# Optimization experiments

Measured on AMD Instinct MI355X. Metric: run time of the kernel, lower is better.

## Reference

```python
import jax, jax.numpy as jnp
import numpy as np

B, S, D, H = 2, 2048, 1024, 16
DK = D // H  # 64


def setup_inputs() -> dict:
    key = jax.random.key(0)
    ks = jax.random.split(key, 11)
    scale = 1.0 / np.sqrt(D)
    inp = {
        "x": jax.random.normal(ks[0], (B, S, D), dtype=jnp.float32),
        "z": jax.random.normal(ks[1], (B, S, D), dtype=jnp.float32),
        # causal mask, broadcast over batch and heads; masked_fill where mask==0
        "mask": jnp.tril(jnp.ones((1, 1, S, S), dtype=jnp.int32)),
        "wq_w": jax.random.normal(ks[2], (D, D), dtype=jnp.float32) * scale,
        "wq_b": jax.random.normal(ks[3], (D,), dtype=jnp.float32) * 0.01,
        "wk_w": jax.random.normal(ks[4], (D, D), dtype=jnp.float32) * scale,
        "wk_b": jax.random.normal(ks[5], (D,), dtype=jnp.float32) * 0.01,
        "wv_w": jax.random.normal(ks[6], (D, D), dtype=jnp.float32) * scale,
        "wv_b": jax.random.normal(ks[7], (D,), dtype=jnp.float32) * 0.01,
        "wo_w": jax.random.normal(ks[8], (D, D), dtype=jnp.float32) * scale,
        "wo_b": jax.random.normal(ks[9], (D,), dtype=jnp.float32) * 0.01,
    }
    return inp


def reference(x, z, mask, wq_w, wq_b, wk_w, wk_b, wv_w, wv_b, wo_w, wo_b):
    # torch Linear: y = x @ W.T + b
    q = x @ wq_w.T + wq_b
    k = z @ wk_w.T + wk_b
    # NOTE: faithful to source bug: value uses wk, not wv (wv is a dead param)
    v = z @ wk_w.T + wk_b

    def split_heads(t):  # [B,S,D] -> [B,H,S,DK]
        return t.reshape(B, S, H, DK).transpose(0, 2, 1, 3)

    q, k, v = split_heads(q), split_heads(k), split_heads(v)

    scores = jnp.einsum("bhqd,bhkd->bhqk", q, k) * (DK ** -0.5)
    scores = jnp.where(mask == 0, -jnp.inf, scores)
    attn_weights = jax.nn.softmax(scores, axis=-1)  # [B,H,S,S]
    atn = jnp.einsum("bhqk,bhkd->bhqd", attn_weights, v)

    concat = atn.transpose(0, 2, 1, 3).reshape(B, S, D)
    output = concat @ wo_w.T + wo_b  # dropout rate 0.0 -> identity
    concat_attn_weight = attn_weights.sum(axis=1)  # [B,S,S]
    return output, concat_attn_weight
```

## Files before the change

### kernel.cpp

```cpp
#include <hip/hip_runtime.h>

typedef __bf16 bf16_t;
typedef __bf16 bf16x4 __attribute__((ext_vector_type(4)));
typedef __bf16 bf16x8 __attribute__((ext_vector_type(8)));
typedef float  f32x4  __attribute__((ext_vector_type(4)));

#define MFMA(a, b, c) __builtin_amdgcn_mfma_f32_16x16x32_bf16((a), (b), (c), 0, 0, 0)

static constexpr int Bsz = 2, S = 2048, D = 1024, H = 16, DK = 64;
#define QSCALE 0.18033688011112042f

__global__ __launch_bounds__(256) void cvt5(
    const float* __restrict__ x, const float* __restrict__ z,
    const float* __restrict__ wq, const float* __restrict__ wk,
    const float* __restrict__ wo,
    bf16_t* __restrict__ xb, bf16_t* __restrict__ zb,
    bf16_t* __restrict__ wqb, bf16_t* __restrict__ wkb, bf16_t* __restrict__ wob)
{
    constexpr int NXZ = Bsz * S * D / 4;
    constexpr int NW  = D * D / 4;
    int i = blockIdx.x * 256 + threadIdx.x;
    const float* s; bf16_t* d; int off;
    if (i < NXZ)                 { s = x;  d = xb;  off = i; }
    else if (i < 2 * NXZ)        { s = z;  d = zb;  off = i - NXZ; }
    else if (i < 2 * NXZ + NW)   { s = wq; d = wqb; off = i - 2 * NXZ; }
    else if (i < 2 * NXZ + 2*NW) { s = wk; d = wkb; off = i - 2 * NXZ - NW; }
    else                         { s = wo; d = wob; off = i - 2 * NXZ - 2 * NW; }
    float4 v = *(const float4*)&s[(size_t)off * 4];
    bf16x4 o;
    o[0] = (bf16_t)v.x; o[1] = (bf16_t)v.y; o[2] = (bf16_t)v.z; o[3] = (bf16_t)v.w;
    *(bf16x4*)&d[(size_t)off * 4] = o;
}

__global__ __launch_bounds__(512) void gemm_qk(
    const bf16_t* __restrict__ xA, const bf16_t* __restrict__ wqB,
    const float* __restrict__ wqb, bf16_t* __restrict__ Qc,
    const bf16_t* __restrict__ zA, const bf16_t* __restrict__ wkB,
    const float* __restrict__ wkb, bf16_t* __restrict__ Kc,
    bf16_t* __restrict__ KTout)
{
    constexpr int N = D, K = D;
    const int zi = blockIdx.z;
    const bf16_t* A    = zi ? zA  : xA;
    const bf16_t* B    = zi ? wkB : wqB;
    const float*  bias = zi ? wkb : wqb;
    bf16_t*       C    = zi ? Kc  : Qc;
    const float   sc   = zi ? 1.f : QSCALE;

    __shared__ bf16_t As[2][128][40];
    __shared__ bf16_t Bs[2][128][40];

    const int t    = threadIdx.x;
    const int wave = t >> 6, lane = t & 63;
    const int quad = lane >> 4, l15 = lane & 15;
    const int wm = (wave >> 1) * 32, wn = (wave & 1) * 64;
    const int rowbase = blockIdx.y * 128, colbase = blockIdx.x * 128;
    const int r  = t >> 2;
    const int cc = (t & 3) << 3;

    f32x4 acc[2][4];
#pragma unroll
    for (int i = 0; i < 2; ++i)
#pragma unroll
        for (int j = 0; j < 4; ++j) acc[i][j] = {0.f, 0.f, 0.f, 0.f};

    bf16x8 areg = *(const bf16x8*)&A[(size_t)(rowbase + r) * K + cc];
    bf16x8 breg = *(const bf16x8*)&B[(size_t)(colbase + r) * K + cc];
    *(bf16x8*)&As[0][r][cc] = areg;
    *(bf16x8*)&Bs[0][r][cc] = breg;
    __syncthreads();

    for (int kt = 0; kt < K; kt += 32) {
        const int cur = (kt >> 5) & 1, nxt = cur ^ 1;
        const bool more = (kt + 32) < K;
        if (more) {
            areg = *(const bf16x8*)&A[(size_t)(rowbase + r) * K + kt + 32 + cc];
            breg = *(const bf16x8*)&B[(size_t)(colbase + r) * K + kt + 32 + cc];
        }

        bf16x8 af[2], bfr[4];
#pragma unroll
        for (int mt = 0; mt < 2; ++mt)
            af[mt] = *(const bf16x8*)&As[cur][wm + mt * 16 + l15][quad * 8];
#pragma unroll
        for (int nt = 0; nt < 4; ++nt)
            bfr[nt] = *(const bf16x8*)&Bs[cur][wn + nt * 16 + l15][quad * 8];
#pragma unroll
        for (int mt = 0; mt < 2; ++mt)
#pragma unroll
            for (int nt = 0; nt < 4; ++nt)
                acc[mt][nt] = MFMA(af[mt], bfr[nt], acc[mt][nt]);

        if (more) {
            *(bf16x8*)&As[nxt][r][cc] = areg;
            *(bf16x8*)&Bs[nxt][r][cc] = breg;
        }
        __syncthreads();
    }

#pragma unroll
    for (int nt = 0; nt < 4; ++nt) {
        int col  = colbase + wn + nt * 16 + l15;
        float bv = bias[col];
#pragma unroll
        for (int mt = 0; mt < 2; ++mt) {
            int row0 = rowbase + wm + mt * 16 + quad * 4;
#pragma unroll
            for (int rr = 0; rr < 4; ++rr) {
                float v = (acc[mt][nt][rr] + bv) * sc;
                C[(size_t)(row0 + rr) * N + col] = (bf16_t)v;
                if (zi) {
                    int row = row0 + rr;
                    int bb = row >> 11, srow = row & (S - 1);
                    int hh = col >> 6,  dd   = col & 63;
                    KTout[(((size_t)bb * H + hh) * DK + dd) * S + srow] = (bf16_t)v;
                }
            }
        }
    }
}

__global__ __launch_bounds__(256) void gemm_obt(
    const bf16_t* __restrict__ A, const bf16_t* __restrict__ B,
    const float* __restrict__ bias, float* __restrict__ C)
{
    constexpr int N = D, K = D;
    __shared__ bf16_t As[2][64][40];
    __shared__ bf16_t Bs[2][128][40];

    const int t    = threadIdx.x;
    const int wave = t >> 6, lane = t & 63;
    const int quad = lane >> 4, l15 = lane & 15;
    const int wm = (wave >> 1) * 32, wn = (wave & 1) * 64;
    const int rowbase = blockIdx.y * 64, colbase = blockIdx.x * 128;
    const int r  = t >> 2;
    const int cc = (t & 3) << 3;

    f32x4 acc[2][4];
#pragma unroll
    for (int i = 0; i < 2; ++i)
#pragma unroll
        for (int j = 0; j < 4; ++j) acc[i][j] = {0.f, 0.f, 0.f, 0.f};

    bf16x8 areg = *(const bf16x8*)&A[(size_t)(rowbase + r) * K + cc];
    bf16x8 breg0 = *(const bf16x8*)&B[(size_t)(colbase + r) * K + cc];
    bf16x8 breg1 = *(const bf16x8*)&B[(size_t)(colbase + 64 + r) * K + cc];
    *(bf16x8*)&As[0][r][cc]      = areg;
    *(bf16x8*)&Bs[0][r][cc]      = breg0;
    *(bf16x8*)&Bs[0][64 + r][cc] = breg1;
    __syncthreads();

    for (int kt = 0; kt < K; kt += 32) {
        const int cur = (kt >> 5) & 1, nxt = cur ^ 1;
        const bool more = (kt + 32) < K;
        if (more) {
            areg  = *(const bf16x8*)&A[(size_t)(rowbase + r) * K + kt + 32 + cc];
            breg0 = *(const bf16x8*)&B[(size_t)(colbase + r) * K + kt + 32 + cc];
            breg1 = *(const bf16x8*)&B[(size_t)(colbase + 64 + r) * K + kt + 32 + cc];
        }

        bf16x8 af[2], bfr[4];
#pragma unroll
        for (int mt = 0; mt < 2; ++mt)
            af[mt] = *(const bf16x8*)&As[cur][wm + mt * 16 + l15][quad * 8];
#pragma unroll
        for (int nt = 0; nt < 4; ++nt)
            bfr[nt] = *(const bf16x8*)&Bs[cur][wn + nt * 16 + l15][quad * 8];
#pragma unroll
        for (int mt = 0; mt < 2; ++mt)
#pragma unroll
            for (int nt = 0; nt < 4; ++nt)
                acc[mt][nt] = MFMA(af[mt], bfr[nt], acc[mt][nt]);

        if (more) {
            *(bf16x8*)&As[nxt][r][cc]      = areg;
            *(bf16x8*)&Bs[nxt][r][cc]      = breg0;
            *(bf16x8*)&Bs[nxt][64 + r][cc] = breg1;
        }
        __syncthreads();
    }

#pragma unroll
    for (int nt = 0; nt < 4; ++nt) {
        int col  = colbase + wn + nt * 16 + l15;
        float bv = bias[col];
#pragma unroll
        for (int mt = 0; mt < 2; ++mt) {
            int row0 = rowbase + wm + mt * 16 + quad * 4;
#pragma unroll
            for (int rr = 0; rr < 4; ++rr)
                C[(size_t)(row0 + rr) * N + col] = acc[mt][nt][rr] + bv;
        }
    }
}

__global__ __launch_bounds__(256) void attn_flash(
    const bf16_t* __restrict__ Q, const bf16_t* __restrict__ Km,
    const bf16_t* __restrict__ KT,
    bf16_t* __restrict__ Oc, float* __restrict__ m_ws, float* __restrict__ il_ws)
{
    const int h = blockIdx.y, b = blockIdx.z;
    const int t = threadIdx.x;
    const int wave = t >> 6, lane = t & 63;
    const int quad = lane >> 4, l15 = lane & 15;

    __shared__ bf16_t Ks[2][64][72];
    __shared__ bf16_t KTs[2][64][72];
    __shared__ bf16_t PQ[64][72];

    const int hcol = h * DK;
    const bf16_t* KTh = KT + ((size_t)(b * H + h)) * DK * S;
    const size_t bS = (size_t)b * S;

    const int jr = (t >> 3);
    const int ce = (t & 7) * 8;
    const int iloc = wave * 16 + l15;

    for (int half = 0; half < 2; ++half) {
        const int qt = half == 0 ? (int)blockIdx.x : 31 - (int)blockIdx.x;
        const size_t qrow0 = bS + (size_t)qt * 64;

        __syncthreads();
        bf16x8 qld[2], kreg[2], ktreg[2];
#pragma unroll
        for (int p = 0; p < 2; ++p) {
            qld[p]   = *(const bf16x8*)&Q[(qrow0 + p * 32 + jr) * D + hcol + ce];
            kreg[p]  = *(const bf16x8*)&Km[(bS + p * 32 + jr) * D + hcol + ce];
            ktreg[p] = *(const bf16x8*)&KTh[(size_t)(p * 32 + jr) * S + ce];
        }
#pragma unroll
        for (int p = 0; p < 2; ++p) {
            *(bf16x8*)&PQ[p * 32 + jr][ce]     = qld[p];
            *(bf16x8*)&Ks[0][p * 32 + jr][ce]  = kreg[p];
            *(bf16x8*)&KTs[0][p * 32 + jr][ce] = ktreg[p];
        }
        __syncthreads();
        const bf16x8 qf0 = *(const bf16x8*)&PQ[wave * 16 + l15][quad * 8];
        const bf16x8 qf1 = *(const bf16x8*)&PQ[wave * 16 + l15][32 + quad * 8];

        f32x4 accO[4];
#pragma unroll
        for (int u = 0; u < 4; ++u) accO[u] = {0.f, 0.f, 0.f, 0.f};
        float m_cur = -1e30f, l_cur = 0.f;

        auto softmax_pv = [&](f32x4 sv[4], int cur) {
            float tm = sv[0][0];
#pragma unroll
            for (int nt = 0; nt < 4; ++nt)
#pragma unroll
                for (int r = 0; r < 4; ++r) tm = fmaxf(tm, sv[nt][r]);
            tm = fmaxf(tm, __shfl_xor(tm, 16));
            tm = fmaxf(tm, __shfl_xor(tm, 32));
            if (__any(tm > m_cur + 8.f)) {
                float m_new = fmaxf(m_cur, tm);
                float alpha = exp2f(m_cur - m_new);
                m_cur = m_new;
                l_cur *= alpha;
                float alpha4[4];
#pragma unroll
                for (int r = 0; r < 4; ++r)
                    alpha4[r] = __shfl(alpha, (quad << 4) + quad * 4 + r, 64);
#pragma unroll
                for (int u = 0; u < 4; ++u)
#pragma unroll
                    for (int r = 0; r < 4; ++r) accO[u][r] *= alpha4[r];
            }
            float rs = 0.f;
#pragma unroll
            for (int nt = 0; nt < 4; ++nt)
#pragma unroll
                for (int r = 0; r < 4; ++r) {
                    float p = exp2f(sv[nt][r] - m_cur);
                    sv[nt][r] = p;
                    rs += p;
                }
            rs += __shfl_xor(rs, 16);
            rs += __shfl_xor(rs, 32);
            l_cur += rs;

#pragma unroll
            for (int nt = 0; nt < 4; ++nt) {
                bf16x4 pk;
                pk[0] = (bf16_t)sv[nt][0]; pk[1] = (bf16_t)sv[nt][1];
                pk[2] = (bf16_t)sv[nt][2]; pk[3] = (bf16_t)sv[nt][3];
                *(bf16x4*)&PQ[wave * 16 + l15][nt * 16 + quad * 4] = pk;
            }
            asm volatile("s_waitcnt lgkmcnt(0)" ::: "memory");

            bf16x8 pa0 = *(const bf16x8*)&PQ[wave * 16 + l15][quad * 8];
            bf16x8 pa1 = *(const bf16x8*)&PQ[wave * 16 + l15][32 + quad * 8];
            __builtin_amdgcn_s_setprio(1);
#pragma unroll
            for (int u = 0; u < 4; ++u) {
                bf16x8 v0 = *(const bf16x8*)&KTs[cur][u * 16 + l15][quad * 8];
                bf16x8 v1 = *(const bf16x8*)&KTs[cur][u * 16 + l15][32 + quad * 8];
                accO[u] = MFMA(pa0, v0, accO[u]);
                accO[u] = MFMA(pa1, v1, accO[u]);
            }
            __builtin_amdgcn_s_setprio(0);
        };

        for (int jt = 0; jt < qt; ++jt) {
            const int cur = jt & 1, nxt = cur ^ 1;
#pragma unroll
            for (int p = 0; p < 2; ++p) {
                kreg[p]  = *(const bf16x8*)&Km[(bS + (size_t)(jt + 1) * 64 + p * 32 + jr) * D + hcol + ce];
                ktreg[p] = *(const bf16x8*)&KTh[(size_t)(p * 32 + jr) * S + (size_t)(jt + 1) * 64 + ce];
            }

            f32x4 sv[4];
            __builtin_amdgcn_s_setprio(1);
#pragma unroll
            for (int nt = 0; nt < 4; ++nt) {
                bf16x8 a0 = *(const bf16x8*)&Ks[cur][nt * 16 + l15][quad * 8];
                bf16x8 a1 = *(const bf16x8*)&Ks[cur][nt * 16 + l15][32 + quad * 8];
                f32x4 a = {0.f, 0.f, 0.f, 0.f};
                a = MFMA(a0, qf0, a);
                a = MFMA(a1, qf1, a);
                sv[nt] = a;
            }
            __builtin_amdgcn_s_setprio(0);
            softmax_pv(sv, cur);

#pragma unroll
            for (int p = 0; p < 2; ++p) {
                *(bf16x8*)&Ks[nxt][p * 32 + jr][ce]  = kreg[p];
                *(bf16x8*)&KTs[nxt][p * 32 + jr][ce] = ktreg[p];
            }
            __syncthreads();
        }

        {
            const int cur = qt & 1;
            f32x4 sv[4];
            __builtin_amdgcn_s_setprio(1);
#pragma unroll
            for (int nt = 0; nt < 4; ++nt) {
                bf16x8 a0 = *(const bf16x8*)&Ks[cur][nt * 16 + l15][quad * 8];
                bf16x8 a1 = *(const bf16x8*)&Ks[cur][nt * 16 + l15][32 + quad * 8];
                f32x4 a = {0.f, 0.f, 0.f, 0.f};
                a = MFMA(a0, qf0, a);
                a = MFMA(a1, qf1, a);
#pragma unroll
                for (int r = 0; r < 4; ++r)
                    if ((nt * 16 + quad * 4 + r) > iloc) a[r] = -1e30f;
                sv[nt] = a;
            }
            __builtin_amdgcn_s_setprio(0);
            softmax_pv(sv, cur);
        }

        float invl = 1.f / l_cur;
        float invl4[4];
#pragma unroll
        for (int r = 0; r < 4; ++r)
            invl4[r] = __shfl(invl, (quad << 4) + quad * 4 + r, 64);
#pragma unroll
        for (int u = 0; u < 4; ++u)
#pragma unroll
            for (int r = 0; r < 4; ++r)
                Oc[(qrow0 + wave * 16 + quad * 4 + r) * D + hcol + u * 16 + l15] =
                    (bf16_t)(accO[u][r] * invl4[r]);

        if (quad == 0) {
            size_t sb = ((size_t)(b * H + h)) * S + (size_t)qt * 64 + wave * 16 + l15;
            m_ws[sb]  = m_cur;
            il_ws[sb] = invl;
        }
    }
}

__global__ __launch_bounds__(256) void attn_wsum(
    const bf16_t* __restrict__ Q, const bf16_t* __restrict__ Km,
    const float* __restrict__ m_ws, const float* __restrict__ il_ws,
    float* __restrict__ out2)
{
    const int jt = blockIdx.x, qt = blockIdx.y, b = blockIdx.z;
    const int t  = threadIdx.x;
    float* tile = out2 + (size_t)b * S * S + (size_t)qt * 64 * S + (size_t)jt * 64;

    if (jt > qt) {
        int r0 = t >> 2, c0 = (t & 3) * 16;
#pragma unroll
        for (int e = 0; e < 16; ++e) tile[(size_t)r0 * S + c0 + e] = 0.f;
        return;
    }

    const int wave = t >> 6, lane = t & 63;
    const int quad = lane >> 4, l15 = lane & 15;
    __shared__ bf16_t Ks[2][64][72];
    __shared__ bf16_t Qs[2][64][72];

    const int jr = (t >> 3), ce = (t & 7) * 8;
    const size_t krow = (size_t)b * S + (size_t)jt * 64;
    const size_t qrow = (size_t)b * S + (size_t)qt * 64;

    f32x4 accs[4];
#pragma unroll
    for (int nt = 0; nt < 4; ++nt) accs[nt] = {0.f, 0.f, 0.f, 0.f};

    bf16x8 kreg[2], qreg[2];
#pragma unroll
    for (int p = 0; p < 2; ++p) {
        kreg[p] = *(const bf16x8*)&Km[(krow + p * 32 + jr) * D + ce];
        qreg[p] = *(const bf16x8*)&Q[(qrow + p * 32 + jr) * D + ce];
    }
#pragma unroll
    for (int p = 0; p < 2; ++p) {
        *(bf16x8*)&Ks[0][p * 32 + jr][ce] = kreg[p];
        *(bf16x8*)&Qs[0][p * 32 + jr][ce] = qreg[p];
    }
    __syncthreads();

    const size_t mlb0 = (size_t)(b * H) * S + (size_t)qt * 64 + wave * 16 + quad * 4;

    if (jt < qt) {
        for (int h = 0; h < H; ++h) {
            const int cur = h & 1, nxt = cur ^ 1;
            if (h < H - 1) {
                const int hc = (h + 1) * DK;
#pragma unroll
                for (int p = 0; p < 2; ++p) {
                    kreg[p] = *(const bf16x8*)&Km[(krow + p * 32 + jr) * D + hc + ce];
                    qreg[p] = *(const bf16x8*)&Q[(qrow + p * 32 + jr) * D + hc + ce];
                }
            }

            bf16x8 qf0 = *(const bf16x8*)&Qs[cur][wave * 16 + l15][quad * 8];
            bf16x8 qf1 = *(const bf16x8*)&Qs[cur][wave * 16 + l15][32 + quad * 8];
            f32x4 mr = *(const f32x4*)&m_ws[mlb0 + (size_t)h * S];
            f32x4 il = *(const f32x4*)&il_ws[mlb0 + (size_t)h * S];

#pragma unroll
            for (int nt = 0; nt < 4; ++nt) {
                bf16x8 k0 = *(const bf16x8*)&Ks[cur][nt * 16 + l15][quad * 8];
                bf16x8 k1 = *(const bf16x8*)&Ks[cur][nt * 16 + l15][32 + quad * 8];
                f32x4 a = {0.f, 0.f, 0.f, 0.f};
                a = MFMA(qf0, k0, a);
                a = MFMA(qf1, k1, a);
#pragma unroll
                for (int r = 0; r < 4; ++r)
                    accs[nt][r] = fmaf(exp2f(a[r] - mr[r]), il[r], accs[nt][r]);
            }

            if (h < H - 1) {
#pragma unroll
                for (int p = 0; p < 2; ++p) {
                    *(bf16x8*)&Ks[nxt][p * 32 + jr][ce] = kreg[p];
                    *(bf16x8*)&Qs[nxt][p * 32 + jr][ce] = qreg[p];
                }
            }
            __syncthreads();
        }
    } else {
        for (int h = 0; h < H; ++h) {
            const int cur = h & 1, nxt = cur ^ 1;
            if (h < H - 1) {
                const int hc = (h + 1) * DK;
#pragma unroll
                for (int p = 0; p < 2; ++p) {
                    kreg[p] = *(const bf16x8*)&Km[(krow + p * 32 + jr) * D + hc + ce];
                    qreg[p] = *(const bf16x8*)&Q[(qrow + p * 32 + jr) * D + hc + ce];
                }
            }

            bf16x8 qf0 = *(const bf16x8*)&Qs[cur][wave * 16 + l15][quad * 8];
            bf16x8 qf1 = *(const bf16x8*)&Qs[cur][wave * 16 + l15][32 + quad * 8];
            f32x4 mr = *(const f32x4*)&m_ws[mlb0 + (size_t)h * S];
            f32x4 il = *(const f32x4*)&il_ws[mlb0 + (size_t)h * S];

#pragma unroll
            for (int nt = 0; nt < 4; ++nt) {
                bf16x8 k0 = *(const bf16x8*)&Ks[cur][nt * 16 + l15][quad * 8];
                bf16x8 k1 = *(const bf16x8*)&Ks[cur][nt * 16 + l15][32 + quad * 8];
                f32x4 a = {0.f, 0.f, 0.f, 0.f};
                a = MFMA(qf0, k0, a);
                a = MFMA(qf1, k1, a);
#pragma unroll
                for (int r = 0; r < 4; ++r) {
                    int i = wave * 16 + quad * 4 + r;
                    int j = nt * 16 + l15;
                    float p = (j <= i) ? exp2f(a[r] - mr[r]) * il[r] : 0.f;
                    accs[nt][r] += p;
                }
            }

            if (h < H - 1) {
#pragma unroll
                for (int p = 0; p < 2; ++p) {
                    *(bf16x8*)&Ks[nxt][p * 32 + jr][ce] = kreg[p];
                    *(bf16x8*)&Qs[nxt][p * 32 + jr][ce] = qreg[p];
                }
            }
            __syncthreads();
        }
    }

#pragma unroll
    for (int nt = 0; nt < 4; ++nt)
#pragma unroll
        for (int r = 0; r < 4; ++r)
            tile[(size_t)(wave * 16 + quad * 4 + r) * S + nt * 16 + l15] = accs[nt][r];
}

extern "C" void kernel_launch(void* const* d_in, const int* in_sizes, int n_in,
                              void* d_out, int out_size, void* d_ws, size_t ws_size,
                              hipStream_t stream)
{
    const float* x    = (const float*)d_in[0];
    const float* z    = (const float*)d_in[1];
    const float* wq_w = (const float*)d_in[3];
    const float* wq_b = (const float*)d_in[4];
    const float* wk_w = (const float*)d_in[5];
    const float* wk_b = (const float*)d_in[6];
    const float* wo_w = (const float*)d_in[9];
    const float* wo_b = (const float*)d_in[10];

    float* out  = (float*)d_out;
    float* out2 = out + (size_t)Bsz * S * D;

    float*  m_ws  = (float*)d_ws;
    float*  il_ws = m_ws + (size_t)Bsz * H * S;
    bf16_t* Qws   = (bf16_t*)(il_ws + (size_t)Bsz * H * S);
    bf16_t* Kws   = Qws + (size_t)Bsz * S * D;
    bf16_t* wq_bf = Kws + (size_t)Bsz * S * D;
    bf16_t* wk_bf = wq_bf + (size_t)D * D;
    bf16_t* wo_bf = wk_bf + (size_t)D * D;
    bf16_t* xb    = (bf16_t*)out;
    bf16_t* zb    = xb + (size_t)Bsz * S * D;
    bf16_t* Cc    = (bf16_t*)out2;
    bf16_t* KTws  = Cc + (size_t)Bsz * S * D;

    constexpr int CVT_BLOCKS = (2 * (Bsz * S * D / 4) + 3 * (D * D / 4)) / 256;
    cvt5<<<dim3(CVT_BLOCKS), dim3(256), 0, stream>>>(
        x, z, wq_w, wk_w, wo_w, xb, zb, wq_bf, wk_bf, wo_bf);
    gemm_qk<<<dim3(D / 128, (Bsz * S) / 128, 2), dim3(512), 0, stream>>>(
        xb, wq_bf, wq_b, Qws, zb, wk_bf, wk_b, Kws, KTws);
    attn_flash<<<dim3(S / 128, H, Bsz), dim3(256), 0, stream>>>(
        Qws, Kws, KTws, Cc, m_ws, il_ws);
    gemm_obt<<<dim3(D / 128, (Bsz * S) / 64, 1), dim3(256), 0, stream>>>(
        Cc, wo_bf, wo_b, out);
    attn_wsum<<<dim3(S / 64, S / 64, Bsz), dim3(256), 0, stream>>>(
        Qws, Kws, m_ws, il_ws, out2);
}
```

Measured before the change: 271.1 us.

## Process both paired query tiles in one KV sweep sharing loaded K tiles

The flash attention kernel previously handled its two causal-balanced query tiles (qt and 31-qt) one after the other, streaming K/V tiles from global memory twice. It now keeps two sets of accumulators and softmax state and walks the K/V sequence once, computing both tiles' scores from the same shared-memory K tile and running tile A only while it is causally active. This cuts global K/V loads and barriers, at the cost of more registers per thread and a second shared P buffer, which may reduce occupancy.

After: 275.8 us. About the same (+1.7%).

```diff
diff --git a/kernel.cpp b/kernel.cpp
--- a/kernel.cpp
+++ b/kernel.cpp
@@ -206,7 +206,8 @@
 
     __shared__ bf16_t Ks[2][64][72];
     __shared__ bf16_t KTs[2][64][72];
-    __shared__ bf16_t PQ[64][72];
+    __shared__ bf16_t PA[64][72];
+    __shared__ bf16_t PB[64][72];
 
     const int hcol = h * DK;
     const bf16_t* KTh = KT + ((size_t)(b * H + h)) * DK * S;
@@ -216,141 +217,156 @@
     const int ce = (t & 7) * 8;
     const int iloc = wave * 16 + l15;
 
-    for (int half = 0; half < 2; ++half) {
-        const int qt = half == 0 ? (int)blockIdx.x : 31 - (int)blockIdx.x;
-        const size_t qrow0 = bS + (size_t)qt * 64;
-
-        __syncthreads();
-        bf16x8 qld[2], kreg[2], ktreg[2];
-#pragma unroll
-        for (int p = 0; p < 2; ++p) {
-            qld[p]   = *(const bf16x8*)&Q[(qrow0 + p * 32 + jr) * D + hcol + ce];
-            kreg[p]  = *(const bf16x8*)&Km[(bS + p * 32 + jr) * D + hcol + ce];
-            ktreg[p] = *(const bf16x8*)&KTh[(size_t)(p * 32 + jr) * S + ce];
-        }
-#pragma unroll
-        for (int p = 0; p < 2; ++p) {
-            *(bf16x8*)&PQ[p * 32 + jr][ce]     = qld[p];
-            *(bf16x8*)&Ks[0][p * 32 + jr][ce]  = kreg[p];
-            *(bf16x8*)&KTs[0][p * 32 + jr][ce] = ktreg[p];
-        }
-        __syncthreads();
-        const bf16x8 qf0 = *(const bf16x8*)&PQ[wave * 16 + l15][quad * 8];
-        const bf16x8 qf1 = *(const bf16x8*)&PQ[wave * 16 + l15][32 + quad * 8];
-
-        f32x4 accO[4];
-#pragma unroll
-        for (int u = 0; u < 4; ++u) accO[u] = {0.f, 0.f, 0.f, 0.f};
-        float m_cur = -1e30f, l_cur = 0.f;
-
-        auto softmax_pv = [&](f32x4 sv[4], int cur) {
-            float tm = sv[0][0];
-#pragma unroll
-            for (int nt = 0; nt < 4; ++nt)
-#pragma unroll
-                for (int r = 0; r < 4; ++r) tm = fmaxf(tm, sv[nt][r]);
-            tm = fmaxf(tm, __shfl_xor(tm, 16));
-            tm = fmaxf(tm, __shfl_xor(tm, 32));
-            if (__any(tm > m_cur + 8.f)) {
-                float m_new = fmaxf(m_cur, tm);
-                float alpha = exp2f(m_cur - m_new);
-                m_cur = m_new;
-                l_cur *= alpha;
-                float alpha4[4];
-#pragma unroll
-                for (int r = 0; r < 4; ++r)
-                    alpha4[r] = __shfl(alpha, (quad << 4) + quad * 4 + r, 64);
-#pragma unroll
-                for (int u = 0; u < 4; ++u)
-#pragma unroll
-                    for (int r = 0; r < 4; ++r) accO[u][r] *= alpha4[r];
-            }
-            float rs = 0.f;
-#pragma unroll
-            for (int nt = 0; nt < 4; ++nt)
-#pragma unroll
-                for (int r = 0; r < 4; ++r) {
-                    float p = exp2f(sv[nt][r] - m_cur);
-                    sv[nt][r] = p;
-                    rs += p;
-                }
-            rs += __shfl_xor(rs, 16);
-            rs += __shfl_xor(rs, 32);
-            l_cur += rs;
-
-#pragma unroll
-            for (int nt = 0; nt < 4; ++nt) {
-                bf16x4 pk;
-                pk[0] = (bf16_t)sv[nt][0]; pk[1] = (bf16_t)sv[nt][1];
-                pk[2] = (bf16_t)sv[nt][2]; pk[3] = (bf16_t)sv[nt][3];
-                *(bf16x4*)&PQ[wave * 16 + l15][nt * 16 + quad * 4] = pk;
-            }
-            asm volatile("s_waitcnt lgkmcnt(0)" ::: "memory");
-
-            bf16x8 pa0 = *(const bf16x8*)&PQ[wave * 16 + l15][quad * 8];
-            bf16x8 pa1 = *(const bf16x8*)&PQ[wave * 16 + l15][32 + quad * 8];
-            __builtin_amdgcn_s_setprio(1);
-#pragma unroll
-            for (int u = 0; u < 4; ++u) {
-                bf16x8 v0 = *(const bf16x8*)&KTs[cur][u * 16 + l15][quad * 8];
-                bf16x8 v1 = *(const bf16x8*)&KTs[cur][u * 16 + l15][32 + quad * 8];
-                accO[u] = MFMA(pa0, v0, accO[u]);
-                accO[u] = MFMA(pa1, v1, accO[u]);
-            }
-            __builtin_amdgcn_s_setprio(0);
-        };
-
-        for (int jt = 0; jt < qt; ++jt) {
-            const int cur = jt & 1, nxt = cur ^ 1;
+    const int qtA = (int)blockIdx.x;
+    const int qtB = 31 - qtA;
+    const size_t qrowA = bS + (size_t)qtA * 64;
+    const size_t qrowB = bS + (size_t)qtB * 64;
+
+    bf16x8 qldA[2], qldB[2], kreg[2], ktreg[2];
+#pragma unroll
+    for (int p = 0; p < 2; ++p) {
+        qldA[p]  = *(const bf16x8*)&Q[(qrowA + p * 32 + jr) * D + hcol + ce];
+        qldB[p]  = *(const bf16x8*)&Q[(qrowB + p * 32 + jr) * D + hcol + ce];
+        kreg[p]  = *(const bf16x8*)&Km[(bS + p * 32 + jr) * D + hcol + ce];
+        ktreg[p] = *(const bf16x8*)&KTh[(size_t)(p * 32 + jr) * S + ce];
+    }
+#pragma unroll
+    for (int p = 0; p < 2; ++p) {
+        *(bf16x8*)&PA[p * 32 + jr][ce]     = qldA[p];
+        *(bf16x8*)&PB[p * 32 + jr][ce]     = qldB[p];
+        *(bf16x8*)&Ks[0][p * 32 + jr][ce]  = kreg[p];
+        *(bf16x8*)&KTs[0][p * 32 + jr][ce] = ktreg[p];
+    }
+    __syncthreads();
+    const bf16x8 qfA0 = *(const bf16x8*)&PA[wave * 16 + l15][quad * 8];
+    const bf16x8 qfA1 = *(const bf16x8*)&PA[wave * 16 + l15][32 + quad * 8];
+    const bf16x8 qfB0 = *(const bf16x8*)&PB[wave * 16 + l15][quad * 8];
+    const bf16x8 qfB1 = *(const bf16x8*)&PB[wave * 16 + l15][32 + quad * 8];
+
+    f32x4 accA[4], accB[4];
+#pragma unroll
+    for (int u = 0; u < 4; ++u) { accA[u] = {0.f, 0.f, 0.f, 0.f}; accB[u] = {0.f, 0.f, 0.f, 0.f}; }
+    float mA = -1e30f, lA = 0.f, mB = -1e30f, lB = 0.f;
+
+    auto softmax_pv = [&](f32x4 (&sv)[4], int cur, float& m_cur, float& l_cur,
+                          f32x4 (&accO)[4], bf16_t (&P)[64][72]) {
+        float tm = sv[0][0];
+#pragma unroll
+        for (int nt = 0; nt < 4; ++nt)
+#pragma unroll
+            for (int r = 0; r < 4; ++r) tm = fmaxf(tm, sv[nt][r]);
+        tm = fmaxf(tm, __shfl_xor(tm, 16));
+        tm = fmaxf(tm, __shfl_xor(tm, 32));
+        if (__any(tm > m_cur + 8.f)) {
+            float m_new = fmaxf(m_cur, tm);
+            float alpha = exp2f(m_cur - m_new);
+            m_cur = m_new;
+            l_cur *= alpha;
+            float alpha4[4];
+#pragma unroll
+            for (int r = 0; r < 4; ++r)
+                alpha4[r] = __shfl(alpha, (quad << 4) + quad * 4 + r, 64);
+#pragma unroll
+            for (int u = 0; u < 4; ++u)
+#pragma unroll
+                for (int r = 0; r < 4; ++r) accO[u][r] *= alpha4[r];
+        }
+        float rs = 0.f;
+#pragma unroll
+        for (int nt = 0; nt < 4; ++nt)
+#pragma unroll
+            for (int r = 0; r < 4; ++r) {
+                float p = exp2f(sv[nt][r] - m_cur);
+                sv[nt][r] = p;
+                rs += p;
+            }
+        rs += __shfl_xor(rs, 16);
+        rs += __shfl_xor(rs, 32);
+        l_cur += rs;
+
+#pragma unroll
+        for (int nt = 0; nt < 4; ++nt) {
+            bf16x4 pk;
+            pk[0] = (bf16_t)sv[nt][0]; pk[1] = (bf16_t)sv[nt][1];
+            pk[2] = (bf16_t)sv[nt][2]; pk[3] = (bf16_t)sv[nt][3];
+            *(bf16x4*)&P[wave * 16 + l15][nt * 16 + quad * 4] = pk;
+        }
+        asm volatile("s_waitcnt lgkmcnt(0)" ::: "memory");
+
+        bf16x8 pa0 = *(const bf16x8*)&P[wave * 16 + l15][quad * 8];
+        bf16x8 pa1 = *(const bf16x8*)&P[wave * 16 + l15][32 + quad * 8];
+        __builtin_amdgcn_s_setprio(1);
+#pragma unroll
+        for (int u = 0; u < 4; ++u) {
+            bf16x8 v0 = *(const bf16x8*)&KTs[cur][u * 16 + l15][quad * 8];
+            bf16x8 v1 = *(const bf16x8*)&KTs[cur][u * 16 + l15][32 + quad * 8];
+            accO[u] = MFMA(pa0, v0, accO[u]);
+            accO[u] = MFMA(pa1, v1, accO[u]);
+        }
+        __builtin_amdgcn_s_setprio(0);
+    };
+
+    for (int jt = 0; jt <= qtB; ++jt) {
+        const int cur = jt & 1, nxt = cur ^ 1;
+        const bool more = jt < qtB;
+        if (more) {
 #pragma unroll
             for (int p = 0; p < 2; ++p) {
                 kreg[p]  = *(const bf16x8*)&Km[(bS + (size_t)(jt + 1) * 64 + p * 32 + jr) * D + hcol + ce];
                 ktreg[p] = *(const bf16x8*)&KTh[(size_t)(p * 32 + jr) * S + (size_t)(jt + 1) * 64 + ce];
             }
-
-            f32x4 sv[4];
-            __builtin_amdgcn_s_setprio(1);
-#pragma unroll
-            for (int nt = 0; nt < 4; ++nt) {
-                bf16x8 a0 = *(const bf16x8*)&Ks[cur][nt * 16 + l15][quad * 8];
-                bf16x8 a1 = *(const bf16x8*)&Ks[cur][nt * 16 + l15][32 + quad * 8];
-                f32x4 a = {0.f, 0.f, 0.f, 0.f};
-                a = MFMA(a0, qf0, a);
-                a = MFMA(a1, qf1, a);
-                sv[nt] = a;
-            }
-            __builtin_amdgcn_s_setprio(0);
-            softmax_pv(sv, cur);
-
+        }
+        const bool actA = jt <= qtA;
+
+        f32x4 svA[4], svB[4];
+        __builtin_amdgcn_s_setprio(1);
+#pragma unroll
+        for (int nt = 0; nt < 4; ++nt) {
+            bf16x8 a0 = *(const bf16x8*)&Ks[cur][nt * 16 + l15][quad * 8];
+            bf16x8 a1 = *(const bf16x8*)&Ks[cur][nt * 16 + l15][32 + quad * 8];
+            f32x4 sb = {0.f, 0.f, 0.f, 0.f};
+            sb = MFMA(a0, qfB0, sb);
+            sb = MFMA(a1, qfB1, sb);
+            svB[nt] = sb;
+            if (actA) {
+                f32x4 sa = {0.f, 0.f, 0.f, 0.f};
+                sa = MFMA(a0, qfA0, sa);
+                sa = MFMA(a1, qfA1, sa);
+                svA[nt] = sa;
+            }
+        }
+        __builtin_amdgcn_s_setprio(0);
+
+        if (jt == qtB) {
+#pragma unroll
+            for (int nt = 0; nt < 4; ++nt)
+#pragma unroll
+                for (int r = 0; r < 4; ++r)
+                    if ((nt * 16 + quad * 4 + r) > iloc) svB[nt][r] = -1e30f;
+        }
+        if (actA && jt == qtA) {
+#pragma unroll
+            for (int nt = 0; nt < 4; ++nt)
+#pragma unroll
+                for (int r = 0; r < 4; ++r)
+                    if ((nt * 16 + quad * 4 + r) > iloc) svA[nt][r] = -1e30f;
+        }
+
+        softmax_pv(svB, cur, mB, lB, accB, PB);
+        if (actA) softmax_pv(svA, cur, mA, lA, accA, PA);
+
+        if (more) {
 #pragma unroll
             for (int p = 0; p < 2; ++p) {
                 *(bf16x8*)&Ks[nxt][p * 32 + jr][ce]  = kreg[p];
                 *(bf16x8*)&KTs[nxt][p * 32 + jr][ce] = ktreg[p];
             }
-            __syncthreads();
-        }
-
-        {
-            const int cur = qt & 1;
-            f32x4 sv[4];
-            __builtin_amdgcn_s_setprio(1);
-#pragma unroll
-            for (int nt = 0; nt < 4; ++nt) {
-                bf16x8 a0 = *(const bf16x8*)&Ks[cur][nt * 16 + l15][quad * 8];
-                bf16x8 a1 = *(const bf16x8*)&Ks[cur][nt * 16 + l15][32 + quad * 8];
-                f32x4 a = {0.f, 0.f, 0.f, 0.f};
-                a = MFMA(a0, qf0, a);
-                a = MFMA(a1, qf1, a);
-#pragma unroll
-                for (int r = 0; r < 4; ++r)
-                    if ((nt * 16 + quad * 4 + r) > iloc) a[r] = -1e30f;
-                sv[nt] = a;
-            }
-            __builtin_amdgcn_s_setprio(0);
-            softmax_pv(sv, cur);
-        }
-
-        float invl = 1.f / l_cur;
+        }
+        __syncthreads();
+    }
+
+    {
+        float invl = 1.f / lB;
         float invl4[4];
 #pragma unroll
         for (int r = 0; r < 4; ++r)
@@ -359,12 +375,29 @@
         for (int u = 0; u < 4; ++u)
 #pragma unroll
             for (int r = 0; r < 4; ++r)
-                Oc[(qrow0 + wave * 16 + quad * 4 + r) * D + hcol + u * 16 + l15] =
-                    (bf16_t)(accO[u][r] * invl4[r]);
-
+                Oc[(qrowB + wave * 16 + quad * 4 + r) * D + hcol + u * 16 + l15] =
+                    (bf16_t)(accB[u][r] * invl4[r]);
         if (quad == 0) {
-            size_t sb = ((size_t)(b * H + h)) * S + (size_t)qt * 64 + wave * 16 + l15;
-            m_ws[sb]  = m_cur;
+            size_t sb = ((size_t)(b * H + h)) * S + (size_t)qtB * 64 + wave * 16 + l15;
+            m_ws[sb]  = mB;
+            il_ws[sb] = invl;
+        }
+    }
+    {
+        float invl = 1.f / lA;
+        float invl4[4];
+#pragma unroll
+        for (int r = 0; r < 4; ++r)
+            invl4[r] = __shfl(invl, (quad << 4) + quad * 4 + r, 64);
+#pragma unroll
+        for (int u = 0; u < 4; ++u)
+#pragma unroll
+            for (int r = 0; r < 4; ++r)
+                Oc[(qrowA + wave * 16 + quad * 4 + r) * D + hcol + u * 16 + l15] =
+                    (bf16_t)(accA[u][r] * invl4[r]);
+        if (quad == 0) {
+            size_t sb = ((size_t)(b * H + h)) * S + (size_t)qtA * 64 + wave * 16 + l15;
+            m_ws[sb]  = mA;
             il_ws[sb] = invl;
         }
     }
```
